# Kernel optimization log

Measured on AMD Instinct MI355X. Metric: run time of the kernel, lower is better.

Reference implementation:

```python
import jax, jax.numpy as jnp
import numpy as np

N_UNITS = 1024
H = 8
D_K = N_UNITS // H
B, NCH, T = 4, 2, 1024


def setup_inputs() -> dict:
    key = jax.random.key(0)
    ks = jax.random.split(key, 9)
    s = 1.0 / np.sqrt(N_UNITS)
    inp = {
        "x": jax.random.normal(ks[0], (B, NCH, T, N_UNITS), dtype=jnp.float32),
        "batch_size": B,
        "Wq": jax.random.uniform(ks[1], (N_UNITS, N_UNITS), jnp.float32, -s, s),
        "bq": jax.random.uniform(ks[2], (N_UNITS,), jnp.float32, -s, s),
        "Wk": jax.random.uniform(ks[3], (N_UNITS, N_UNITS), jnp.float32, -s, s),
        "bk": jax.random.uniform(ks[4], (N_UNITS,), jnp.float32, -s, s),
        "Wv": jax.random.uniform(ks[5], (N_UNITS, N_UNITS), jnp.float32, -s, s),
        "bv": jax.random.uniform(ks[6], (N_UNITS,), jnp.float32, -s, s),
        "Wo": jax.random.uniform(ks[7], (N_UNITS, N_UNITS), jnp.float32, -s, s),
        "bo": jax.random.uniform(ks[8], (N_UNITS,), jnp.float32, -s, s),
    }
    return inp


def reference(x, batch_size, Wq, bq, Wk, bk, Wv, bv, Wo, bo):
    # x: [B, nch, T, n_units] (the 4D co-attention path)
    nch = x.shape[1]
    dk_co = D_K * nch  # _d_k in the original
    # Linear is y = x @ W.T + b
    q = jnp.einsum("bntu,vu->bntv", x, Wq) + bq  # [B,nch,T,U]
    k = jnp.einsum("bntu,vu->bntv", x, Wk) + bk
    v = jnp.einsum("bntu,vu->bntv", x, Wv) + bv
    # transpose(1,2) then reshape(B,-1,h,nch*d_k): [B,T,nch,U] -> [B,T,H,nch*d_k]
    q = jnp.transpose(q, (0, 2, 1, 3)).reshape(batch_size, -1, H, dk_co)
    k = jnp.transpose(k, (0, 2, 1, 3)).reshape(batch_size, -1, H, dk_co)
    # v: reshape(B, nch, -1, h, d_k) -> [B,nch,T,H,d_k]
    v = v.reshape(batch_size, nch, -1, H, D_K)
    # scores: [B,H,T,T], scaled by sqrt(nch*d_k)
    scores = jnp.einsum("bthd,bshd->bhts", q, k) / np.sqrt(dk_co)
    att = jax.nn.softmax(scores, axis=-1)  # dropout is identity in eval
    # expand of att across nch is implicit in the einsum (no materialized expand)
    out = jnp.einsum("bhts,bnshd->bnthd", att, v)  # [B,nch,T,H,d_k]
    out = out.reshape(batch_size, nch, -1, H * D_K)
    return jnp.einsum("bntu,vu->bntv", out, Wo) + bo
```

## Files before the change

kernel.cpp:

```cpp
#include <hip/hip_runtime.h>
#include <cstdint>
#include <cstddef>


typedef __bf16 bf16_t;
typedef __attribute__((ext_vector_type(8))) __bf16 bf16x8;
typedef __attribute__((ext_vector_type(4))) __bf16 bf16x4;
typedef __attribute__((ext_vector_type(4))) float f32x4;

__device__ __forceinline__ void async_copy16(const bf16_t* g, bf16_t* l) {
  auto* gp = reinterpret_cast<const __attribute__((address_space(1))) void*>(
      reinterpret_cast<uintptr_t>(g));
  auto* lp = reinterpret_cast<__attribute__((address_space(3))) void*>(
      reinterpret_cast<uintptr_t>(l));
  __builtin_amdgcn_global_load_lds(gp, lp, 16, 0, 0);
}

__device__ __forceinline__ void cast8(const float* s, bf16_t* d) {
  const float4 a = ((const float4*)s)[0];
  const float4 b = ((const float4*)s)[1];
  bf16x8 o;
  o[0] = (bf16_t)a.x; o[1] = (bf16_t)a.y; o[2] = (bf16_t)a.z; o[3] = (bf16_t)a.w;
  o[4] = (bf16_t)b.x; o[5] = (bf16_t)b.y; o[6] = (bf16_t)b.z; o[7] = (bf16_t)b.w;
  *(bf16x8*)d = o;
}

__global__ void cast_all(const float* __restrict__ x,
                         const float* __restrict__ Wq,
                         const float* __restrict__ Wk,
                         const float* __restrict__ Wv,
                         const float* __restrict__ Wo, bf16_t* __restrict__ xb,
                         bf16_t* __restrict__ wqkv, bf16_t* __restrict__ wob) {
  const int i = blockIdx.x * blockDim.x + threadIdx.x;
  if (i < 1048576) {
    cast8(x + (size_t)i * 8, xb + (size_t)i * 8);
  } else {
    const int j = i - 1048576;
    if (j < 393216) {
      const int seg = j >> 17;
      const float* w = (seg == 0) ? Wq : ((seg == 1) ? Wk : Wv);
      cast8(w + (size_t)(j - seg * 131072) * 8, wqkv + (size_t)j * 8);
    } else if (j < 524288) {
      cast8(Wo + (size_t)(j - 393216) * 8, wob + (size_t)(j - 393216) * 8);
    }
  }
}

__global__ __launch_bounds__(256, 2) void gemm_qkv(
    const bf16_t* __restrict__ A, const bf16_t* __restrict__ W,
    const float* __restrict__ bq, const float* __restrict__ bk,
    const float* __restrict__ bv, bf16_t* __restrict__ qb,
    bf16_t* __restrict__ kb, bf16_t* __restrict__ vtb, float qscale) {
  __shared__ bf16_t sA[128 * 64];
  __shared__ bf16_t sB[128 * 64];
  const int tid = threadIdx.x;
  const int w = tid >> 6;
  const int lane = tid & 63;
  const int l15 = lane & 15;
  const int quad = lane >> 4;
  const int wm = (w >> 1) * 64;
  const int wn = (w & 1) * 64;
  const int m0 = blockIdx.x * 128;
  const int n0 = blockIdx.y * 128;
  const int K = 1024;

  const int srow = lane >> 3;
  const int sgrp = (lane & 7) ^ srow;
  const bf16_t* aB = A + (size_t)(m0 + srow) * K + sgrp * 8;
  const bf16_t* bB = W + (size_t)(n0 + srow) * K + sgrp * 8;

  f32x4 acc[4][4];
#pragma unroll
  for (int i = 0; i < 4; ++i)
#pragma unroll
    for (int j = 0; j < 4; ++j) acc[i][j] = (f32x4){0.f, 0.f, 0.f, 0.f};

  for (int kt = 0; kt < K; kt += 64) {
#pragma unroll
    for (int i = 0; i < 4; ++i) {
      const int c = w * 4 + i;
      async_copy16(aB + (size_t)(c * 8) * K + kt, &sA[c * 512]);
      async_copy16(bB + (size_t)(c * 8) * K + kt, &sB[c * 512]);
    }
    __syncthreads();
#pragma unroll
    for (int ks = 0; ks < 2; ++ks) {
      bf16x8 af[4], bfv[4];
#pragma unroll
      for (int mi = 0; mi < 4; ++mi) {
        const int row = wm + mi * 16 + l15;
        const int grp = ks * 4 + quad;
        af[mi] = *(const bf16x8*)&sA[row * 64 + ((grp ^ (row & 7)) << 3)];
      }
#pragma unroll
      for (int ni = 0; ni < 4; ++ni) {
        const int row = wn + ni * 16 + l15;
        const int grp = ks * 4 + quad;
        bfv[ni] = *(const bf16x8*)&sB[row * 64 + ((grp ^ (row & 7)) << 3)];
      }
#pragma unroll
      for (int mi = 0; mi < 4; ++mi)
#pragma unroll
        for (int ni = 0; ni < 4; ++ni)
          acc[mi][ni] = __builtin_amdgcn_mfma_f32_16x16x32_bf16(
              af[mi], bfv[ni], acc[mi][ni], 0, 0, 0);
    }
    __syncthreads();
  }

  const int seg = n0 >> 10;
  const float scale = (seg == 0) ? qscale : 1.0f;
  const float* bp = (seg == 0) ? bq : ((seg == 1) ? bk : bv);
  float bvr[4];
#pragma unroll
  for (int ni = 0; ni < 4; ++ni)
    bvr[ni] = bp[(n0 + wn + ni * 16 + l15) & 1023];

  if (seg < 2) {
    bf16_t* out = (seg == 0) ? qb : kb;
#pragma unroll
    for (int mi = 0; mi < 4; ++mi) {
      const int rowb = m0 + wm + mi * 16 + quad * 4;
#pragma unroll
      for (int ni = 0; ni < 4; ++ni) {
        const int col = (n0 + wn + ni * 16 + l15) & 1023;
#pragma unroll
        for (int r = 0; r < 4; ++r)
          out[(size_t)(rowb + r) * 1024 + col] =
              (bf16_t)((acc[mi][ni][r] + bvr[ni]) * scale);
      }
    }
  } else {
#pragma unroll
    for (int mi = 0; mi < 4; ++mi) {
      const int rowb = m0 + wm + mi * 16 + quad * 4;
      const int bn = rowb >> 10;
      const int t = rowb & 1023;
#pragma unroll
      for (int ni = 0; ni < 4; ++ni) {
        const int u = (n0 + wn + ni * 16 + l15) & 1023;
        bf16x4 v4;
#pragma unroll
        for (int r = 0; r < 4; ++r) v4[r] = (bf16_t)(acc[mi][ni][r] + bvr[ni]);
        *(bf16x4*)&vtb[((size_t)(bn * 1024 + u)) * 1024 + t] = v4;
      }
    }
  }
}

__global__ __launch_bounds__(256, 2) void gemm_out(
    const bf16_t* __restrict__ A, const bf16_t* __restrict__ W,
    const float* __restrict__ bias, float* __restrict__ Cout) {
  __shared__ bf16_t sA[128 * 64];
  __shared__ bf16_t sB[128 * 64];
  const int tid = threadIdx.x;
  const int w = tid >> 6;
  const int lane = tid & 63;
  const int l15 = lane & 15;
  const int quad = lane >> 4;
  const int wm = (w >> 1) * 64;
  const int wn = (w & 1) * 64;
  const int m0 = blockIdx.x * 128;
  const int n0 = blockIdx.y * 128;
  const int K = 1024, N = 1024;

  const int srow = lane >> 3;
  const int sgrp = (lane & 7) ^ srow;
  const bf16_t* aB = A + (size_t)(m0 + srow) * K + sgrp * 8;
  const bf16_t* bB = W + (size_t)(n0 + srow) * K + sgrp * 8;

  f32x4 acc[4][4];
#pragma unroll
  for (int i = 0; i < 4; ++i)
#pragma unroll
    for (int j = 0; j < 4; ++j) acc[i][j] = (f32x4){0.f, 0.f, 0.f, 0.f};

  for (int kt = 0; kt < K; kt += 64) {
#pragma unroll
    for (int i = 0; i < 4; ++i) {
      const int c = w * 4 + i;
      async_copy16(aB + (size_t)(c * 8) * K + kt, &sA[c * 512]);
      async_copy16(bB + (size_t)(c * 8) * K + kt, &sB[c * 512]);
    }
    __syncthreads();
#pragma unroll
    for (int ks = 0; ks < 2; ++ks) {
      bf16x8 af[4], bfv[4];
#pragma unroll
      for (int mi = 0; mi < 4; ++mi) {
        const int row = wm + mi * 16 + l15;
        const int grp = ks * 4 + quad;
        af[mi] = *(const bf16x8*)&sA[row * 64 + ((grp ^ (row & 7)) << 3)];
      }
#pragma unroll
      for (int ni = 0; ni < 4; ++ni) {
        const int row = wn + ni * 16 + l15;
        const int grp = ks * 4 + quad;
        bfv[ni] = *(const bf16x8*)&sB[row * 64 + ((grp ^ (row & 7)) << 3)];
      }
#pragma unroll
      for (int mi = 0; mi < 4; ++mi)
#pragma unroll
        for (int ni = 0; ni < 4; ++ni)
          acc[mi][ni] = __builtin_amdgcn_mfma_f32_16x16x32_bf16(
              af[mi], bfv[ni], acc[mi][ni], 0, 0, 0);
    }
    __syncthreads();
  }

  float bvr[4];
#pragma unroll
  for (int ni = 0; ni < 4; ++ni) bvr[ni] = bias[n0 + wn + ni * 16 + l15];
#pragma unroll
  for (int mi = 0; mi < 4; ++mi) {
    const int rowb = m0 + wm + mi * 16 + quad * 4;
#pragma unroll
    for (int ni = 0; ni < 4; ++ni) {
      const int col = n0 + wn + ni * 16 + l15;
#pragma unroll
      for (int r = 0; r < 4; ++r)
        Cout[(size_t)(rowb + r) * N + col] = acc[mi][ni][r] + bvr[ni];
    }
  }
}

__global__ __launch_bounds__(256, 2) void attention_k(
    const bf16_t* __restrict__ qb, const bf16_t* __restrict__ kb,
    const bf16_t* __restrict__ vtb, bf16_t* __restrict__ ob) {
  __shared__ bf16_t sK[64 * 256];
  __shared__ bf16_t sV[256 * 64];
  __shared__ bf16_t sP[64 * 72];
  __shared__ float sL[2][64];
  const int tid = threadIdx.x;
  const int w = tid >> 6;
  const int lane = tid & 63;
  const int l15 = lane & 15;
  const int quad = lane >> 4;
  const int qt = blockIdx.x, h = blockIdx.y, b = blockIdx.z;
  const int t0 = qt * 64;
  const int qm = (w & 1) * 32;
  const int sOff = (w >> 1) * 32;
  const int uOff = (w >> 1) * 128;
  const size_t qkrow0 =
      ((size_t)(b * 2 + (h >> 2)) * 1024) * 1024 + (h & 3) * 256;

  bf16x8 qf[2][8];
#pragma unroll
  for (int m = 0; m < 2; ++m) {
    const bf16_t* qrow =
        qb + qkrow0 + (size_t)(t0 + qm + m * 16 + l15) * 1024 + quad * 8;
#pragma unroll
    for (int kk = 0; kk < 8; ++kk)
      qf[m][kk] = *(const bf16x8*)(qrow + kk * 32);
  }

  f32x4 o[2][8];
#pragma unroll
  for (int m = 0; m < 2; ++m)
#pragma unroll
    for (int ct = 0; ct < 8; ++ct) o[m][ct] = (f32x4){0.f, 0.f, 0.f, 0.f};
  float lsum[2] = {0.f, 0.f};

  const int krow_l = w * 2 + (lane >> 5);
  const int kslot = lane & 31;
  const int vrow_l = w * 8 + (lane >> 3);
  const int vslot = lane & 7;

  for (int st = 0; st < 16; ++st) {
    __syncthreads();
#pragma unroll
    for (int r = 0; r < 8; ++r) {
      const int lr = r * 8 + krow_l;
      const int g = kslot ^ (lr & 7);
      async_copy16(kb + qkrow0 + (size_t)(st * 64 + lr) * 1024 + g * 8,
                   &sK[(r * 8 + w * 2) * 256]);
    }
#pragma unroll
    for (int r = 0; r < 8; ++r) {
      const int c = r * 32 + vrow_l;
      const int g = vslot ^ (c & 7);
      async_copy16(
          vtb +
              ((size_t)(b * 2 + (c >> 7)) * 1024 + h * 128 + (c & 127)) * 1024 +
              st * 64 + g * 8,
          &sV[(r * 32 + w * 8) * 64]);
    }
    __syncthreads();

    f32x4 s4[2][2];
#pragma unroll
    for (int m = 0; m < 2; ++m)
#pragma unroll
      for (int nt = 0; nt < 2; ++nt) s4[m][nt] = (f32x4){0.f, 0.f, 0.f, 0.f};
#pragma unroll
    for (int kk = 0; kk < 8; ++kk) {
#pragma unroll
      for (int nt = 0; nt < 2; ++nt) {
        bf16x8 kf = *(const bf16x8*)&sK[(sOff + nt * 16 + l15) * 256 +
                                        (((kk * 4 + quad) ^ (l15 & 7)) << 3)];
#pragma unroll
        for (int m = 0; m < 2; ++m)
          s4[m][nt] = __builtin_amdgcn_mfma_f32_16x16x32_bf16(
              kf, qf[m][kk], s4[m][nt], 0, 0, 0);
      }
    }

#pragma unroll
    for (int m = 0; m < 2; ++m) {
#pragma unroll
      for (int nt = 0; nt < 2; ++nt) {
        bf16x4 p4;
        float ps = 0.f;
#pragma unroll
        for (int r = 0; r < 4; ++r) {
          const float p = __builtin_amdgcn_exp2f(s4[m][nt][r]);
          p4[r] = (bf16_t)p;
          ps += p;
        }
        lsum[m] += ps;
        *(bf16x4*)&sP[(qm + m * 16 + l15) * 72 + sOff + nt * 16 + quad * 4] =
            p4;
      }
    }
    __syncthreads();

#pragma unroll
    for (int kk = 0; kk < 2; ++kk) {
      bf16x8 pf[2];
#pragma unroll
      for (int m = 0; m < 2; ++m)
        pf[m] = *(const bf16x8*)&sP[(qm + m * 16 + l15) * 72 + kk * 32 +
                                    quad * 8];
#pragma unroll
      for (int ct = 0; ct < 8; ++ct) {
        bf16x8 vf = *(const bf16x8*)&sV[(uOff + ct * 16 + l15) * 64 +
                                        (((kk * 4 + quad) ^ (l15 & 7)) << 3)];
#pragma unroll
        for (int m = 0; m < 2; ++m)
          o[m][ct] = __builtin_amdgcn_mfma_f32_16x16x32_bf16(pf[m], vf,
                                                             o[m][ct], 0, 0, 0);
      }
    }
  }

#pragma unroll
  for (int m = 0; m < 2; ++m) {
    float v = lsum[m];
    v += __shfl_xor(v, 16, 64);
    v += __shfl_xor(v, 32, 64);
    if (lane < 16) sL[w >> 1][qm + m * 16 + l15] = v;
  }
  __syncthreads();

#pragma unroll
  for (int m = 0; m < 2; ++m) {
    float rl[4];
#pragma unroll
    for (int r = 0; r < 4; ++r) {
      const int row = qm + m * 16 + quad * 4 + r;
      rl[r] = 1.0f / (sL[0][row] + sL[1][row]);
    }
#pragma unroll
    for (int ct = 0; ct < 8; ++ct) {
      const int u = uOff + ct * 16 + l15;
      const int outc = h * 128 + (u & 127);
      const size_t rbase =
          ((size_t)(b * 2 + (u >> 7)) * 1024 + t0 + qm + m * 16 + quad * 4) *
              1024 +
          outc;
#pragma unroll
      for (int r = 0; r < 4; ++r)
        ob[rbase + (size_t)r * 1024] = (bf16_t)(o[m][ct][r] * rl[r]);
    }
  }
}

extern "C" void kernel_launch(void* const* d_in, const int* in_sizes, int n_in,
                              void* d_out, int out_size, void* d_ws,
                              size_t ws_size, hipStream_t stream) {
  const float* x = (const float*)d_in[0];
  const float* Wq = (const float*)d_in[2];
  const float* bq = (const float*)d_in[3];
  const float* Wk = (const float*)d_in[4];
  const float* bk = (const float*)d_in[5];
  const float* Wv = (const float*)d_in[6];
  const float* bv = (const float*)d_in[7];
  const float* Wo = (const float*)d_in[8];
  const float* bo = (const float*)d_in[9];
  float* out = (float*)d_out;

  char* ws = (char*)d_ws;
  const size_t MB = 1u << 20;
  bf16_t* xb = (bf16_t*)(ws);
  bf16_t* qb = (bf16_t*)(ws + 16 * MB);
  bf16_t* kb = (bf16_t*)(ws + 32 * MB);
  bf16_t* vtb = (bf16_t*)(ws + 48 * MB);
  bf16_t* wqkv = (bf16_t*)(ws + 64 * MB);
  bf16_t* wob = (bf16_t*)(ws + 70 * MB);
  bf16_t* ob = xb;

  cast_all<<<6144, 256, 0, stream>>>(x, Wq, Wk, Wv, Wo, xb, wqkv, wob);

  gemm_qkv<<<dim3(64, 24), 256, 0, stream>>>(
      xb, wqkv, bq, bk, bv, qb, kb, vtb, 0.0625f * 1.4426950408889634f);

  attention_k<<<dim3(16, 8, 4), 256, 0, stream>>>(qb, kb, vtb, ob);

  gemm_out<<<dim3(64, 8), 256, 0, stream>>>(ob, wob, bo, out);
}
```

Baseline: 230.6 us.

## Double-buffer weight tiles in LDS and load activations directly to registers

Both projection GEMMs now double-buffer the weight tile in shared memory, prefetching the next K-slice asynchronously while MFMAs run on the current one. The activation tile no longer goes through LDS: each wave loads its A fragments straight from global memory into registers, also prefetched one step ahead. The aim is to hide load latency and cut the two barriers per K-step down to one. In exchange, register pressure rises from two sets of A fragments, and A rows are reloaded from global by both waves that share them instead of being shared through LDS.

```diff
diff --git a/kernel.cpp b/kernel.cpp
--- a/kernel.cpp
+++ b/kernel.cpp
@@ -46,67 +46,81 @@
   }
 }
 
+#define GEMM_STEP(KT, AFC, AFN, SBC, SBN)                                      \
+  {                                                                            \
+    if ((KT) < 15) {                                                           \
+      _Pragma("unroll") for (int i = 0; i < 4; ++i) {                          \
+        const int c = w * 4 + i;                                               \
+        async_copy16(bB + (size_t)(c * 8) * 1024 + ((KT) + 1) * 64,            \
+                     (SBN) + c * 512);                                         \
+      }                                                                        \
+      _Pragma("unroll") for (int mi = 0; mi < 4; ++mi) {                       \
+        _Pragma("unroll") for (int ks = 0; ks < 2; ++ks) {                     \
+          AFN[mi][ks] = *(const bf16x8*)(aF + (size_t)(mi * 16) * 1024 +       \
+                                         ((KT) + 1) * 64 + ks * 32);           \
+        }                                                                      \
+      }                                                                        \
+    }                                                                          \
+    _Pragma("unroll") for (int ks = 0; ks < 2; ++ks) {                         \
+      bf16x8 bfv[4];                                                           \
+      _Pragma("unroll") for (int ni = 0; ni < 4; ++ni) {                       \
+        const int row = wn + ni * 16 + l15;                                    \
+        const int grp = ks * 4 + quad;                                         \
+        bfv[ni] = *(const bf16x8*)&(SBC)[row * 64 + ((grp ^ (row & 7)) << 3)]; \
+      }                                                                        \
+      _Pragma("unroll") for (int mi = 0; mi < 4; ++mi) {                       \
+        _Pragma("unroll") for (int ni = 0; ni < 4; ++ni) {                     \
+          acc[mi][ni] = __builtin_amdgcn_mfma_f32_16x16x32_bf16(               \
+              AFC[mi][ks], bfv[ni], acc[mi][ni], 0, 0, 0);                     \
+        }                                                                      \
+      }                                                                        \
+    }                                                                          \
+    __syncthreads();                                                           \
+  }
+
+#define GEMM_PROLOGUE_AND_LOOP()                                               \
+  const int tid = threadIdx.x;                                                 \
+  const int w = tid >> 6;                                                      \
+  const int lane = tid & 63;                                                   \
+  const int l15 = lane & 15;                                                   \
+  const int quad = lane >> 4;                                                  \
+  const int wm = (w >> 1) * 64;                                                \
+  const int wn = (w & 1) * 64;                                                 \
+  const int m0 = blockIdx.x * 128;                                             \
+  const int n0 = blockIdx.y * 128;                                             \
+  const int srow = lane >> 3;                                                  \
+  const int sgrp = (lane & 7) ^ srow;                                          \
+  const bf16_t* bB = W + (size_t)(n0 + srow) * 1024 + sgrp * 8;                \
+  const bf16_t* aF = A + (size_t)(m0 + wm + l15) * 1024 + quad * 8;            \
+  f32x4 acc[4][4];                                                             \
+  _Pragma("unroll") for (int i = 0; i < 4; ++i) {                              \
+    _Pragma("unroll") for (int j = 0; j < 4; ++j) {                            \
+      acc[i][j] = (f32x4){0.f, 0.f, 0.f, 0.f};                                 \
+    }                                                                          \
+  }                                                                            \
+  bf16x8 af0[4][2], af1[4][2];                                                 \
+  _Pragma("unroll") for (int mi = 0; mi < 4; ++mi) {                           \
+    _Pragma("unroll") for (int ks = 0; ks < 2; ++ks) {                         \
+      af0[mi][ks] = *(const bf16x8*)(aF + (size_t)(mi * 16) * 1024 + ks * 32); \
+    }                                                                          \
+  }                                                                            \
+  _Pragma("unroll") for (int i = 0; i < 4; ++i) {                              \
+    const int c = w * 4 + i;                                                   \
+    async_copy16(bB + (size_t)(c * 8) * 1024, &sB[0][c * 512]);                \
+  }                                                                            \
+  __syncthreads();                                                             \
+  for (int kt = 0; kt < 16; kt += 2) {                                         \
+    GEMM_STEP(kt, af0, af1, &sB[0][0], &sB[1][0]);                             \
+    GEMM_STEP(kt + 1, af1, af0, &sB[1][0], &sB[0][0]);                         \
+  }
+
 __global__ __launch_bounds__(256, 2) void gemm_qkv(
     const bf16_t* __restrict__ A, const bf16_t* __restrict__ W,
     const float* __restrict__ bq, const float* __restrict__ bk,
     const float* __restrict__ bv, bf16_t* __restrict__ qb,
     bf16_t* __restrict__ kb, bf16_t* __restrict__ vtb, float qscale) {
-  __shared__ bf16_t sA[128 * 64];
-  __shared__ bf16_t sB[128 * 64];
-  const int tid = threadIdx.x;
-  const int w = tid >> 6;
-  const int lane = tid & 63;
-  const int l15 = lane & 15;
-  const int quad = lane >> 4;
-  const int wm = (w >> 1) * 64;
-  const int wn = (w & 1) * 64;
-  const int m0 = blockIdx.x * 128;
-  const int n0 = blockIdx.y * 128;
-  const int K = 1024;
-
-  const int srow = lane >> 3;
-  const int sgrp = (lane & 7) ^ srow;
-  const bf16_t* aB = A + (size_t)(m0 + srow) * K + sgrp * 8;
-  const bf16_t* bB = W + (size_t)(n0 + srow) * K + sgrp * 8;
-
-  f32x4 acc[4][4];
-#pragma unroll
-  for (int i = 0; i < 4; ++i)
-#pragma unroll
-    for (int j = 0; j < 4; ++j) acc[i][j] = (f32x4){0.f, 0.f, 0.f, 0.f};
-
-  for (int kt = 0; kt < K; kt += 64) {
-#pragma unroll
-    for (int i = 0; i < 4; ++i) {
-      const int c = w * 4 + i;
-      async_copy16(aB + (size_t)(c * 8) * K + kt, &sA[c * 512]);
-      async_copy16(bB + (size_t)(c * 8) * K + kt, &sB[c * 512]);
-    }
-    __syncthreads();
-#pragma unroll
-    for (int ks = 0; ks < 2; ++ks) {
-      bf16x8 af[4], bfv[4];
-#pragma unroll
-      for (int mi = 0; mi < 4; ++mi) {
-        const int row = wm + mi * 16 + l15;
-        const int grp = ks * 4 + quad;
-        af[mi] = *(const bf16x8*)&sA[row * 64 + ((grp ^ (row & 7)) << 3)];
-      }
-#pragma unroll
-      for (int ni = 0; ni < 4; ++ni) {
-        const int row = wn + ni * 16 + l15;
-        const int grp = ks * 4 + quad;
-        bfv[ni] = *(const bf16x8*)&sB[row * 64 + ((grp ^ (row & 7)) << 3)];
-      }
-#pragma unroll
-      for (int mi = 0; mi < 4; ++mi)
-#pragma unroll
-        for (int ni = 0; ni < 4; ++ni)
-          acc[mi][ni] = __builtin_amdgcn_mfma_f32_16x16x32_bf16(
-              af[mi], bfv[ni], acc[mi][ni], 0, 0, 0);
-    }
-    __syncthreads();
-  }
+  __shared__ bf16_t sB[2][128 * 64];
+  GEMM_PROLOGUE_AND_LOOP();
 
   const int seg = n0 >> 10;
   const float scale = (seg == 0) ? qscale : 1.0f;
@@ -151,62 +165,8 @@
 __global__ __launch_bounds__(256, 2) void gemm_out(
     const bf16_t* __restrict__ A, const bf16_t* __restrict__ W,
     const float* __restrict__ bias, float* __restrict__ Cout) {
-  __shared__ bf16_t sA[128 * 64];
-  __shared__ bf16_t sB[128 * 64];
-  const int tid = threadIdx.x;
-  const int w = tid >> 6;
-  const int lane = tid & 63;
-  const int l15 = lane & 15;
-  const int quad = lane >> 4;
-  const int wm = (w >> 1) * 64;
-  const int wn = (w & 1) * 64;
-  const int m0 = blockIdx.x * 128;
-  const int n0 = blockIdx.y * 128;
-  const int K = 1024, N = 1024;
-
-  const int srow = lane >> 3;
-  const int sgrp = (lane & 7) ^ srow;
-  const bf16_t* aB = A + (size_t)(m0 + srow) * K + sgrp * 8;
-  const bf16_t* bB = W + (size_t)(n0 + srow) * K + sgrp * 8;
-
-  f32x4 acc[4][4];
-#pragma unroll
-  for (int i = 0; i < 4; ++i)
-#pragma unroll
-    for (int j = 0; j < 4; ++j) acc[i][j] = (f32x4){0.f, 0.f, 0.f, 0.f};
-
-  for (int kt = 0; kt < K; kt += 64) {
-#pragma unroll
-    for (int i = 0; i < 4; ++i) {
-      const int c = w * 4 + i;
-      async_copy16(aB + (size_t)(c * 8) * K + kt, &sA[c * 512]);
-      async_copy16(bB + (size_t)(c * 8) * K + kt, &sB[c * 512]);
-    }
-    __syncthreads();
-#pragma unroll
-    for (int ks = 0; ks < 2; ++ks) {
-      bf16x8 af[4], bfv[4];
-#pragma unroll
-      for (int mi = 0; mi < 4; ++mi) {
-        const int row = wm + mi * 16 + l15;
-        const int grp = ks * 4 + quad;
-        af[mi] = *(const bf16x8*)&sA[row * 64 + ((grp ^ (row & 7)) << 3)];
-      }
-#pragma unroll
-      for (int ni = 0; ni < 4; ++ni) {
-        const int row = wn + ni * 16 + l15;
-        const int grp = ks * 4 + quad;
-        bfv[ni] = *(const bf16x8*)&sB[row * 64 + ((grp ^ (row & 7)) << 3)];
-      }
-#pragma unroll
-      for (int mi = 0; mi < 4; ++mi)
-#pragma unroll
-        for (int ni = 0; ni < 4; ++ni)
-          acc[mi][ni] = __builtin_amdgcn_mfma_f32_16x16x32_bf16(
-              af[mi], bfv[ni], acc[mi][ni], 0, 0, 0);
-    }
-    __syncthreads();
-  }
+  __shared__ bf16_t sB[2][128 * 64];
+  GEMM_PROLOGUE_AND_LOOP();
 
   float bvr[4];
 #pragma unroll
@@ -219,7 +179,7 @@
       const int col = n0 + wn + ni * 16 + l15;
 #pragma unroll
       for (int r = 0; r < 4; ++r)
-        Cout[(size_t)(rowb + r) * N + col] = acc[mi][ni][r] + bvr[ni];
+        Cout[(size_t)(rowb + r) * 1024 + col] = acc[mi][ni][r] + bvr[ni];
     }
   }
 }
```

Result: slower. 307.5 us (+33.4%).
